# Optimization experiments

Hardware: AMD Instinct MI355X
Metric: run time of the kernel (lower is better)

## Reference

```python
import jax, jax.numpy as jnp
import numpy as np

D = 768          # hidden_size
M = 8            # num_patchmerges
B = 16
S = 2048         # non-CLF tokens


def setup_inputs() -> dict:
    key = jax.random.key(0)
    ks = jax.random.split(key, 12)
    std = 0.02
    tokens = jax.random.normal(ks[0], (B, 1 + S, D), dtype=jnp.float32)
    lengths = jnp.maximum(jax.random.randint(ks[1], (B,), 0, S), 1).astype(jnp.int64)
    # PatchMerger: learned queries + layernorm params
    q = jax.random.normal(ks[2], (M, D), dtype=jnp.float32) * std
    ln_scale = jnp.ones((D,), dtype=jnp.float32)
    ln_bias = jnp.zeros((D,), dtype=jnp.float32)
    # mlp1: Linear(3D, D) -> GELU -> Linear(D, D)
    w1a = jax.random.normal(ks[3], (3 * D, D), dtype=jnp.float32) * std
    b1a = jnp.zeros((D,), dtype=jnp.float32)
    w2a = jax.random.normal(ks[4], (D, D), dtype=jnp.float32) * std
    b2a = jnp.zeros((D,), dtype=jnp.float32)
    # mlp2: Linear((1+M)D, D) -> GELU -> Linear(D, D)
    w1b = jax.random.normal(ks[5], ((1 + M) * D, D), dtype=jnp.float32) * std
    b1b = jnp.zeros((D,), dtype=jnp.float32)
    w2b = jax.random.normal(ks[6], (D, D), dtype=jnp.float32) * std
    b2b = jnp.zeros((D,), dtype=jnp.float32)
    return dict(tokens=tokens, lengths=lengths, q=q, ln_scale=ln_scale,
                ln_bias=ln_bias, w1a=w1a, b1a=b1a, w2a=w2a, b2a=b2a,
                w1b=w1b, b1b=b1b, w2b=w2b, b2b=b2b)


def _hpmlp(x, w1, b1, w2, b2):
    h = jax.nn.gelu(x @ w1 + b1, approximate=False)  # dropout=0 -> identity
    return h @ w2 + b2


def _layernorm(x, scale, bias, eps=1e-5):
    mu = jnp.mean(x, axis=-1, keepdims=True)
    var = jnp.var(x, axis=-1, keepdims=True)
    return (x - mu) * jax.lax.rsqrt(var + eps) * scale + bias


def reference(tokens, lengths, q, ln_scale, ln_bias,
              w1a, b1a, w2a, b2a, w1b, b1b, w2b, b2b):
    clf = tokens[:, 0]            # [B, D]
    x = tokens[:, 1:]             # [B, S, D]
    mask = jnp.arange(S)[None, :] < lengths[:, None]   # [B, S]
    mf = mask[..., None].astype(x.dtype)

    # fixed path: masked mean / max / min over valid tokens
    denom = lengths.astype(x.dtype)[:, None]
    mean_p = jnp.sum(x * mf, axis=1) / denom
    max_p = jnp.max(jnp.where(mask[..., None], x, -jnp.inf), axis=1)
    min_p = jnp.min(jnp.where(mask[..., None], x, jnp.inf), axis=1)
    pooled_trad = jnp.concatenate([mean_p, max_p, min_p], axis=-1)  # [B, 3D]
    out_fixed = _hpmlp(pooled_trad, w1a, b1a, w2a, b2a)

    # learned path: PatchMerger (masked attention from M learned queries)
    xn = _layernorm(x, ln_scale, ln_bias)
    scores = jnp.einsum('md,bsd->bms', q, xn) / jnp.sqrt(jnp.asarray(D, x.dtype))
    scores = jnp.where(mask[:, None, :], scores, -jnp.inf)
    attn = jax.nn.softmax(scores, axis=-1)                # [B, M, S]
    merged = jnp.einsum('bms,bsd->bmd', attn, x)          # [B, M, D]
    pooled_learn = jnp.concatenate([merged.reshape(B, M * D), clf], axis=-1)
    out_learn = _hpmlp(pooled_learn, w1b, b1b, w2b, b2b)

    return jnp.concatenate([out_fixed, out_learn], axis=-1)  # [B, 2D]
```

## Files before the change

### kernel.cpp

```cpp
#include <hip/hip_runtime.h>
#include <math.h>

#define SD 768
#define SB 16
#define SM 8
#define SS 2048
#define TOK_ROW 2049
#define NEG_INF (-__builtin_inff())

#define OFF_PPOOL   0
#define OFF_PO      1179648
#define OFF_PML     4325376
#define OFF_PTRAD   4333568
#define OFF_PLEARN  4370432
#define OFF_P1A     4481024
#define OFF_P1B     4702208
#define OFF_P2A     5390336
#define OFF_P2B     5464064

__device__ __forceinline__ int clen(int v) { return v < 1 ? 1 : (v > SS ? SS : v); }

__global__ __launch_bounds__(256, 1) void k1_flash(
    const float* __restrict__ tokens, const int* __restrict__ lengths,
    const float* __restrict__ q, const float* __restrict__ lns,
    const float* __restrict__ lnb, float* __restrict__ ppool,
    float* __restrict__ pO, float* __restrict__ pml) {
  int c = blockIdx.x, b = blockIdx.y;
  int len = clen(lengths[b]);
  int c0 = c * 64;
  if (c0 >= len) return;
  int tid = threadIdx.x, w = tid >> 6, lane = tid & 63;
  int mm = lane & 7;

  __shared__ float pool_lds[4][3][SD];
  __shared__ float O_lds[SM][SD];
  __shared__ float l_lds[4][8];

  float4 qr[8][3];
  float qs1sel, qbsel;
  {
    float4 l4[3], lb4[3];
    #pragma unroll
    for (int g = 0; g < 3; ++g) {
      l4[g] = *(const float4*)(lns + g * 256 + lane * 4);
      lb4[g] = *(const float4*)(lnb + g * 256 + lane * 4);
    }
    float qs1r[8], qbr[8];
    #pragma unroll
    for (int m = 0; m < 8; ++m) {
      float s1 = 0.f, sb = 0.f;
      #pragma unroll
      for (int g = 0; g < 3; ++g) {
        float4 qv = *(const float4*)(q + m * SD + g * 256 + lane * 4);
        float4 qs;
        qs.x = qv.x * l4[g].x; qs.y = qv.y * l4[g].y;
        qs.z = qv.z * l4[g].z; qs.w = qv.w * l4[g].w;
        qr[m][g] = qs;
        s1 += qs.x + qs.y + qs.z + qs.w;
        sb += qv.x * lb4[g].x + qv.y * lb4[g].y + qv.z * lb4[g].z + qv.w * lb4[g].w;
      }
      #pragma unroll
      for (int o = 32; o; o >>= 1) { s1 += __shfl_xor(s1, o, 64); sb += __shfl_xor(sb, o, 64); }
      qs1r[m] = s1; qbr[m] = sb;
    }
    qs1sel = qs1r[0]; qbsel = qbr[0];
    #pragma unroll
    for (int m = 1; m < 8; ++m) {
      qs1sel = (mm == m) ? qs1r[m] : qs1sel;
      qbsel = (mm == m) ? qbr[m] : qbsel;
    }
  }

  float psum[12], pmax[12], pmin[12];
  #pragma unroll
  for (int j = 0; j < 12; ++j) { psum[j] = 0.f; pmax[j] = NEG_INF; pmin[j] = -NEG_INF; }
  float O[8][12];
  #pragma unroll
  for (int m = 0; m < 8; ++m)
    #pragma unroll
    for (int j = 0; j < 12; ++j) O[m][j] = 0.f;
  float lacc = 0.f;

  int srow = c0 + w * 16;
  int smax = len - srow; if (smax > 16) smax = 16; if (smax < 0) smax = 0;
  const float* xrow = tokens + ((size_t)b * TOK_ROW + 1 + srow) * SD;

  float4 a0v = {}, a1v = {}, a2v = {}, b0v = {}, b1v = {}, b2v = {};
  if (smax > 0) {
    a0v = *(const float4*)(xrow + lane * 4);
    a1v = *(const float4*)(xrow + 256 + lane * 4);
    a2v = *(const float4*)(xrow + 512 + lane * 4);
  }
  if (smax > 1) {
    const float* xq = xrow + SD;
    b0v = *(const float4*)(xq + lane * 4);
    b1v = *(const float4*)(xq + 256 + lane * 4);
    b2v = *(const float4*)(xq + 512 + lane * 4);
  }
  for (int i = 0; i < smax; ++i) {
    float4 x0 = a0v, x1 = a1v, x2 = a2v;
    a0v = b0v; a1v = b1v; a2v = b2v;
    if (i + 2 < smax) {
      const float* xq = xrow + (size_t)(i + 2) * SD;
      b0v = *(const float4*)(xq + lane * 4);
      b1v = *(const float4*)(xq + 256 + lane * 4);
      b2v = *(const float4*)(xq + 512 + lane * 4);
    }
    float xv[12] = {x0.x, x0.y, x0.z, x0.w, x1.x, x1.y, x1.z, x1.w,
                    x2.x, x2.y, x2.z, x2.w};
    float s1 = 0.f, s2 = 0.f;
    #pragma unroll
    for (int j = 0; j < 12; ++j) {
      float v = xv[j];
      psum[j] += v;
      pmax[j] = fmaxf(pmax[j], v);
      pmin[j] = fminf(pmin[j], v);
      s1 += v;
      s2 += v * v;
    }
    float d[8];
    #pragma unroll
    for (int m = 0; m < 8; ++m) {
      float4 a0 = qr[m][0], a1 = qr[m][1], a2 = qr[m][2];
      d[m] = a0.x * xv[0] + a0.y * xv[1] + a0.z * xv[2] + a0.w * xv[3]
           + a1.x * xv[4] + a1.y * xv[5] + a1.z * xv[6] + a1.w * xv[7]
           + a2.x * xv[8] + a2.y * xv[9] + a2.z * xv[10] + a2.w * xv[11];
    }
    #pragma unroll
    for (int o = 1; o <= 4; o <<= 1)
      #pragma unroll
      for (int m = 0; m < 8; ++m) d[m] += __shfl_xor(d[m], o, 64);
    float u = d[0];
    #pragma unroll
    for (int m = 1; m < 8; ++m) u = (mm == m) ? d[m] : u;
    #pragma unroll
    for (int o = 8; o <= 32; o <<= 1) {
      u += __shfl_xor(u, o, 64);
      s1 += __shfl_xor(s1, o, 64);
      s2 += __shfl_xor(s2, o, 64);
    }
    #pragma unroll
    for (int o = 1; o <= 4; o <<= 1) { s1 += __shfl_xor(s1, o, 64); s2 += __shfl_xor(s2, o, 64); }
    float mu = s1 * (1.f / 768.f);
    float var = s2 * (1.f / 768.f) - mu * mu;
    float rstd = rsqrtf(var + 1e-5f);
    float sc = (rstd * u - rstd * mu * qs1sel + qbsel) * 0.03608439182435161f;
    float p = __expf(sc);
    lacc += p;
    float pm[8];
    #pragma unroll
    for (int mi = 0; mi < 8; ++mi) pm[mi] = __shfl(p, (lane & 56) | mi, 64);
    #pragma unroll
    for (int m = 0; m < 8; ++m)
      #pragma unroll
      for (int j = 0; j < 12; ++j) O[m][j] += pm[m] * xv[j];
  }

  if (lane < 8) l_lds[w][lane] = lacc;
  #pragma unroll
  for (int g = 0; g < 3; ++g) {
    int dd = g * 256 + lane * 4;
    *(float4*)&pool_lds[w][0][dd] = make_float4(psum[g*4], psum[g*4+1], psum[g*4+2], psum[g*4+3]);
    *(float4*)&pool_lds[w][1][dd] = make_float4(pmax[g*4], pmax[g*4+1], pmax[g*4+2], pmax[g*4+3]);
    *(float4*)&pool_lds[w][2][dd] = make_float4(pmin[g*4], pmin[g*4+1], pmin[g*4+2], pmin[g*4+3]);
  }
  __syncthreads();
  if (tid < 8)
    pml[(size_t)(c * SB + b) * 8 + tid] =
        l_lds[0][tid] + l_lds[1][tid] + l_lds[2][tid] + l_lds[3][tid];

  #pragma unroll
  for (int r = 0; r < 4; ++r) {
    if (w == r) {
      #pragma unroll
      for (int m = 0; m < 8; ++m)
        #pragma unroll
        for (int g = 0; g < 3; ++g) {
          int dd = g * 256 + lane * 4;
          float4 mine = make_float4(O[m][g*4], O[m][g*4+1], O[m][g*4+2], O[m][g*4+3]);
          if (r == 0) {
            *(float4*)&O_lds[m][dd] = mine;
          } else {
            float4 cur = *(float4*)&O_lds[m][dd];
            cur.x += mine.x; cur.y += mine.y; cur.z += mine.z; cur.w += mine.w;
            *(float4*)&O_lds[m][dd] = cur;
          }
        }
    }
    __syncthreads();
  }

  size_t obase = (size_t)(c * SB + b) * 6144;
  const float* of = &O_lds[0][0];
  for (int j = tid * 4; j < 6144; j += 1024)
    *(float4*)&pO[obase + j] = *(const float4*)&of[j];

  size_t pbase = (size_t)(c * SB + b) * 2304;
  for (int j4 = tid * 4; j4 < 2304; j4 += 1024) {
    int stat = j4 / SD, dd = j4 - stat * SD;
    float4 v0 = *(float4*)&pool_lds[0][stat][dd];
    float4 v1 = *(float4*)&pool_lds[1][stat][dd];
    float4 v2 = *(float4*)&pool_lds[2][stat][dd];
    float4 v3 = *(float4*)&pool_lds[3][stat][dd];
    float4 r;
    if (stat == 0) {
      r.x = v0.x + v1.x + v2.x + v3.x; r.y = v0.y + v1.y + v2.y + v3.y;
      r.z = v0.z + v1.z + v2.z + v3.z; r.w = v0.w + v1.w + v2.w + v3.w;
    } else if (stat == 1) {
      r.x = fmaxf(fmaxf(v0.x, v1.x), fmaxf(v2.x, v3.x));
      r.y = fmaxf(fmaxf(v0.y, v1.y), fmaxf(v2.y, v3.y));
      r.z = fmaxf(fmaxf(v0.z, v1.z), fmaxf(v2.z, v3.z));
      r.w = fmaxf(fmaxf(v0.w, v1.w), fmaxf(v2.w, v3.w));
    } else {
      r.x = fminf(fminf(v0.x, v1.x), fminf(v2.x, v3.x));
      r.y = fminf(fminf(v0.y, v1.y), fminf(v2.y, v3.y));
      r.z = fminf(fminf(v0.z, v1.z), fminf(v2.z, v3.z));
      r.w = fminf(fminf(v0.w, v1.w), fminf(v2.w, v3.w));
    }
    *(float4*)&ppool[pbase + j4] = r;
  }
}

__global__ void k_combine(const float* __restrict__ ppool, const float* __restrict__ pO,
                          const float* __restrict__ pml, const float* __restrict__ tokens,
                          const int* __restrict__ lengths,
                          float* __restrict__ ptrad, float* __restrict__ plearn) {
  int tile = blockIdx.x, b = blockIdx.y;
  int len = clen(lengths[b]);
  int nv = (len + 63) >> 6;
  int tid = threadIdx.x;
  __shared__ float l_sh[32][8];
  __shared__ float Linv_lds[8];
  for (int t = tid; t < nv * 8; t += 256)
    l_sh[t >> 3][t & 7] = pml[(size_t)((t >> 3) * SB + b) * 8 + (t & 7)];
  __syncthreads();
  if (tid < 8) {
    float L = 0.f;
    for (int cc = 0; cc < nv; ++cc) L += l_sh[cc][tid];
    Linv_lds[tid] = 1.f / L;
  }
  __syncthreads();
  #pragma unroll
  for (int k = 0; k < 4; ++k) {
    int jj = tile * 1024 + k * 256 + tid;
    if (jj < 2304) {
      int stat = jj / SD;
      const float* pp = ppool + jj + (size_t)b * 2304;
      if (stat == 0) {
        float a0 = 0.f, a1 = 0.f, a2 = 0.f, a3 = 0.f;
        int cc = 0;
        for (; cc + 4 <= nv; cc += 4) {
          a0 += pp[(size_t)(cc    ) * SB * 2304];
          a1 += pp[(size_t)(cc + 1) * SB * 2304];
          a2 += pp[(size_t)(cc + 2) * SB * 2304];
          a3 += pp[(size_t)(cc + 3) * SB * 2304];
        }
        for (; cc < nv; ++cc) a0 += pp[(size_t)cc * SB * 2304];
        ptrad[b * 2304 + jj] = ((a0 + a1) + (a2 + a3)) / (float)len;
      } else if (stat == 1) {
        float a0 = NEG_INF, a1 = NEG_INF, a2 = NEG_INF, a3 = NEG_INF;
        int cc = 0;
        for (; cc + 4 <= nv; cc += 4) {
          a0 = fmaxf(a0, pp[(size_t)(cc    ) * SB * 2304]);
          a1 = fmaxf(a1, pp[(size_t)(cc + 1) * SB * 2304]);
          a2 = fmaxf(a2, pp[(size_t)(cc + 2) * SB * 2304]);
          a3 = fmaxf(a3, pp[(size_t)(cc + 3) * SB * 2304]);
        }
        for (; cc < nv; ++cc) a0 = fmaxf(a0, pp[(size_t)cc * SB * 2304]);
        ptrad[b * 2304 + jj] = fmaxf(fmaxf(a0, a1), fmaxf(a2, a3));
      } else {
        float a0 = -NEG_INF, a1 = -NEG_INF, a2 = -NEG_INF, a3 = -NEG_INF;
        int cc = 0;
        for (; cc + 4 <= nv; cc += 4) {
          a0 = fminf(a0, pp[(size_t)(cc    ) * SB * 2304]);
          a1 = fminf(a1, pp[(size_t)(cc + 1) * SB * 2304]);
          a2 = fminf(a2, pp[(size_t)(cc + 2) * SB * 2304]);
          a3 = fminf(a3, pp[(size_t)(cc + 3) * SB * 2304]);
        }
        for (; cc < nv; ++cc) a0 = fminf(a0, pp[(size_t)cc * SB * 2304]);
        ptrad[b * 2304 + jj] = fminf(fminf(a0, a1), fminf(a2, a3));
      }
    } else if (jj < 8448) {
      int t = jj - 2304;
      int m = t / SD;
      const float* po = pO + t + (size_t)b * 6144;
      float a0 = 0.f, a1 = 0.f, a2 = 0.f, a3 = 0.f;
      float a4 = 0.f, a5 = 0.f, a6 = 0.f, a7 = 0.f;
      int cc = 0;
      for (; cc + 8 <= nv; cc += 8) {
        a0 += po[(size_t)(cc    ) * SB * 6144];
        a1 += po[(size_t)(cc + 1) * SB * 6144];
        a2 += po[(size_t)(cc + 2) * SB * 6144];
        a3 += po[(size_t)(cc + 3) * SB * 6144];
        a4 += po[(size_t)(cc + 4) * SB * 6144];
        a5 += po[(size_t)(cc + 5) * SB * 6144];
        a6 += po[(size_t)(cc + 6) * SB * 6144];
        a7 += po[(size_t)(cc + 7) * SB * 6144];
      }
      for (; cc < nv; ++cc) a0 += po[(size_t)cc * SB * 6144];
      plearn[b * 6912 + t] = (((a0 + a1) + (a2 + a3)) + ((a4 + a5) + (a6 + a7))) * Linv_lds[m];
    } else {
      int dd = jj - 8448;
      plearn[b * 6912 + 6144 + dd] = tokens[(size_t)b * TOK_ROW * SD + dd];
    }
  }
}

__global__ __launch_bounds__(256) void gemm_partial(
    const float* __restrict__ XA, const float* __restrict__ WA, int ktA, float* __restrict__ PA,
    const float* __restrict__ XB, const float* __restrict__ WB, float* __restrict__ PB) {
  int nt = blockIdx.x, ky = blockIdx.y;
  const float *X, *W; float* P; int kt, ktN;
  if (ky < ktA) { X = XA; W = WA; P = PA; kt = ky; ktN = ktA; }
  else { X = XB; W = WB; P = PB; kt = ky - ktA; ktN = gridDim.y - ktA; }
  int K = ktN * 128;
  int k0 = kt * 128;
  __shared__ __align__(16) float xt[128 * 20];
  __shared__ float red[4][64][17];
  int tid = threadIdx.x;
  int kk = tid & 127, half = tid >> 7;
  #pragma unroll
  for (int u = 0; u < 8; ++u) {
    int b2 = half * 8 + u;
    xt[kk * 20 + b2] = X[b2 * K + k0 + kk];
  }
  __syncthreads();
  int w = tid >> 6, lane = tid & 63;
  int n = nt * 64 + lane;
  float acc[16];
  #pragma unroll
  for (int b2 = 0; b2 < 16; ++b2) acc[b2] = 0.f;
  const float* Wp = W + (size_t)k0 * SD + n;
  #pragma unroll 8
  for (int kj = 0; kj < 32; ++kj) {
    int k = w + kj * 4;
    float wv = Wp[(size_t)k * SD];
    const float4* xr = reinterpret_cast<const float4*>(xt + k * 20);
    float4 a0 = xr[0], a1 = xr[1], a2 = xr[2], a3 = xr[3];
    acc[0] += wv * a0.x; acc[1] += wv * a0.y; acc[2] += wv * a0.z; acc[3] += wv * a0.w;
    acc[4] += wv * a1.x; acc[5] += wv * a1.y; acc[6] += wv * a1.z; acc[7] += wv * a1.w;
    acc[8] += wv * a2.x; acc[9] += wv * a2.y; acc[10] += wv * a2.z; acc[11] += wv * a2.w;
    acc[12] += wv * a3.x; acc[13] += wv * a3.y; acc[14] += wv * a3.z; acc[15] += wv * a3.w;
  }
  #pragma unroll
  for (int b2 = 0; b2 < 16; ++b2) red[w][lane][b2] = acc[b2];
  __syncthreads();
  for (int i = tid; i < 1024; i += 256) {
    int nn = i & 63, b2 = i >> 6;
    float r = red[0][nn][b2] + red[1][nn][b2] + red[2][nn][b2] + red[3][nn][b2];
    P[(size_t)(kt * 16 + b2) * SD + nt * 64 + nn] = r;
  }
}

template <int NP>
__device__ __forceinline__ void stage_gelu(const float* __restrict__ P1,
                                           const float* __restrict__ bias,
                                           float* __restrict__ xt, int k0, int tid) {
  int kk = tid & 127, half = tid >> 7;
  #pragma unroll
  for (int u = 0; u < 8; ++u) {
    int b2 = half * 8 + u;
    float r = bias[k0 + kk];
    const float* p = P1 + (size_t)b2 * SD + k0 + kk;
    #pragma unroll
    for (int kt2 = 0; kt2 < NP; ++kt2) r += p[(size_t)kt2 * 12288];
    xt[kk * 20 + b2] = r * 0.5f * (1.f + erff(r * 0.70710678118654752f));
  }
}

__global__ __launch_bounds__(256) void gemm2_gelu(
    const float* __restrict__ P1A, const float* __restrict__ b1a,
    const float* __restrict__ W2A, float* __restrict__ P2A,
    const float* __restrict__ P1B, const float* __restrict__ b1b,
    const float* __restrict__ W2B, float* __restrict__ P2B) {
  int nt = blockIdx.x, ky = blockIdx.y;
  __shared__ __align__(16) float xt[128 * 20];
  __shared__ float red[4][64][17];
  int tid = threadIdx.x;
  const float* W; float* P2; int kt;
  if (ky < 6) { kt = ky; W = W2A; P2 = P2A; stage_gelu<18>(P1A, b1a, xt, kt * 128, tid); }
  else { kt = ky - 6; W = W2B; P2 = P2B; stage_gelu<54>(P1B, b1b, xt, kt * 128, tid); }
  int k0 = kt * 128;
  __syncthreads();
  int w = tid >> 6, lane = tid & 63;
  int n = nt * 64 + lane;
  float acc[16];
  #pragma unroll
  for (int b2 = 0; b2 < 16; ++b2) acc[b2] = 0.f;
  const float* Wp = W + (size_t)k0 * SD + n;
  #pragma unroll 8
  for (int kj = 0; kj < 32; ++kj) {
    int k = w + kj * 4;
    float wv = Wp[(size_t)k * SD];
    const float4* xr = reinterpret_cast<const float4*>(xt + k * 20);
    float4 a0 = xr[0], a1 = xr[1], a2 = xr[2], a3 = xr[3];
    acc[0] += wv * a0.x; acc[1] += wv * a0.y; acc[2] += wv * a0.z; acc[3] += wv * a0.w;
    acc[4] += wv * a1.x; acc[5] += wv * a1.y; acc[6] += wv * a1.z; acc[7] += wv * a1.w;
    acc[8] += wv * a2.x; acc[9] += wv * a2.y; acc[10] += wv * a2.z; acc[11] += wv * a2.w;
    acc[12] += wv * a3.x; acc[13] += wv * a3.y; acc[14] += wv * a3.z; acc[15] += wv * a3.w;
  }
  #pragma unroll
  for (int b2 = 0; b2 < 16; ++b2) red[w][lane][b2] = acc[b2];
  __syncthreads();
  for (int i = tid; i < 1024; i += 256) {
    int nn = i & 63, b2 = i >> 6;
    float r = red[0][nn][b2] + red[1][nn][b2] + red[2][nn][b2] + red[3][nn][b2];
    P2[(size_t)(kt * 16 + b2) * SD + nt * 64 + nn] = r;
  }
}

__global__ void final_reduce(const float* __restrict__ P2A, const float* __restrict__ b2a,
                             const float* __restrict__ P2B, const float* __restrict__ b2b,
                             float* __restrict__ out) {
  int y = blockIdx.y;
  const float* P = y ? P2B : P2A;
  const float* bias = y ? b2b : b2a;
  int j = blockIdx.x * 256 + threadIdx.x;
  float r = bias[j % SD];
  #pragma unroll
  for (int kt = 0; kt < 6; ++kt) r += P[kt * 12288 + j];
  int b = j / SD, nn = j - b * SD;
  out[b * 1536 + y * SD + nn] = r;
}

extern "C" void kernel_launch(void* const* d_in, const int* in_sizes, int n_in,
                              void* d_out, int out_size, void* d_ws, size_t ws_size,
                              hipStream_t stream) {
  const float* tokens = (const float*)d_in[0];
  const int* lengths  = (const int*)d_in[1];
  const float* q      = (const float*)d_in[2];
  const float* lns    = (const float*)d_in[3];
  const float* lnb    = (const float*)d_in[4];
  const float* w1a    = (const float*)d_in[5];
  const float* b1a    = (const float*)d_in[6];
  const float* w2a    = (const float*)d_in[7];
  const float* b2a    = (const float*)d_in[8];
  const float* w1b    = (const float*)d_in[9];
  const float* b1b    = (const float*)d_in[10];
  const float* w2b    = (const float*)d_in[11];
  const float* b2b    = (const float*)d_in[12];
  float* ws  = (float*)d_ws;
  float* out = (float*)d_out;

  float* ppool  = ws + OFF_PPOOL;
  float* pO     = ws + OFF_PO;
  float* pml    = ws + OFF_PML;
  float* ptrad  = ws + OFF_PTRAD;
  float* plearn = ws + OFF_PLEARN;
  float* p1a    = ws + OFF_P1A;
  float* p1b    = ws + OFF_P1B;
  float* p2a    = ws + OFF_P2A;
  float* p2b    = ws + OFF_P2B;

  k1_flash<<<dim3(32, 16), 256, 0, stream>>>(tokens, lengths, q, lns, lnb, ppool, pO, pml);
  k_combine<<<dim3(9, 16), 256, 0, stream>>>(ppool, pO, pml, tokens, lengths, ptrad, plearn);
  gemm_partial<<<dim3(12, 72), 256, 0, stream>>>(ptrad, w1a, 18, p1a, plearn, w1b, p1b);
  gemm2_gelu<<<dim3(12, 12), 256, 0, stream>>>(p1a, b1a, w2a, p2a, p1b, b1b, w2b, p2b);
  final_reduce<<<dim3(48, 2), 256, 0, stream>>>(p2a, b2a, p2b, b2b, out);
}
```

Measured before the change: 266.8 us.

## Split flash kernel into score and accumulate passes to raise occupancy

The flash pooling kernel now makes two passes over its tokens. The first pass computes the stats and softmax weights and stores the weights in LDS. The second pass re-reads the tokens and accumulates the weighted sums, so the O accumulators are no longer live while the score math runs. This cuts register pressure, which allows launch_bounds 3 and shares LDS between the pool and O buffers. Chunk size drops from 64 to 32 tokens, doubling the grid and the partial buffers that k_combine reduces, and each token is read twice (the second read likely from cache).

```diff
diff --git a/kernel.cpp b/kernel.cpp
--- a/kernel.cpp
+++ b/kernel.cpp
@@ -9,31 +9,31 @@
 #define NEG_INF (-__builtin_inff())
 
 #define OFF_PPOOL   0
-#define OFF_PO      1179648
-#define OFF_PML     4325376
-#define OFF_PTRAD   4333568
-#define OFF_PLEARN  4370432
-#define OFF_P1A     4481024
-#define OFF_P1B     4702208
-#define OFF_P2A     5390336
-#define OFF_P2B     5464064
+#define OFF_PO      2359296
+#define OFF_PML     8650752
+#define OFF_PTRAD   8658944
+#define OFF_PLEARN  8695808
+#define OFF_P1A     8806400
+#define OFF_P1B     9027584
+#define OFF_P2A     9691136
+#define OFF_P2B     9764864
 
 __device__ __forceinline__ int clen(int v) { return v < 1 ? 1 : (v > SS ? SS : v); }
 
-__global__ __launch_bounds__(256, 1) void k1_flash(
+__global__ __launch_bounds__(256, 3) void k1_flash(
     const float* __restrict__ tokens, const int* __restrict__ lengths,
     const float* __restrict__ q, const float* __restrict__ lns,
     const float* __restrict__ lnb, float* __restrict__ ppool,
     float* __restrict__ pO, float* __restrict__ pml) {
   int c = blockIdx.x, b = blockIdx.y;
   int len = clen(lengths[b]);
-  int c0 = c * 64;
+  int c0 = c * 32;
   if (c0 >= len) return;
   int tid = threadIdx.x, w = tid >> 6, lane = tid & 63;
   int mm = lane & 7;
 
-  __shared__ float pool_lds[4][3][SD];
-  __shared__ float O_lds[SM][SD];
+  __shared__ float buf[4][3][SD];
+  __shared__ float p_lds[4][8][8];
   __shared__ float l_lds[4][8];
 
   float4 qr[8][3];
@@ -74,38 +74,17 @@
   float psum[12], pmax[12], pmin[12];
   #pragma unroll
   for (int j = 0; j < 12; ++j) { psum[j] = 0.f; pmax[j] = NEG_INF; pmin[j] = -NEG_INF; }
-  float O[8][12];
-  #pragma unroll
-  for (int m = 0; m < 8; ++m)
-    #pragma unroll
-    for (int j = 0; j < 12; ++j) O[m][j] = 0.f;
   float lacc = 0.f;
 
-  int srow = c0 + w * 16;
-  int smax = len - srow; if (smax > 16) smax = 16; if (smax < 0) smax = 0;
+  int srow = c0 + w * 8;
+  int smax = len - srow; if (smax > 8) smax = 8; if (smax < 0) smax = 0;
   const float* xrow = tokens + ((size_t)b * TOK_ROW + 1 + srow) * SD;
 
-  float4 a0v = {}, a1v = {}, a2v = {}, b0v = {}, b1v = {}, b2v = {};
-  if (smax > 0) {
-    a0v = *(const float4*)(xrow + lane * 4);
-    a1v = *(const float4*)(xrow + 256 + lane * 4);
-    a2v = *(const float4*)(xrow + 512 + lane * 4);
-  }
-  if (smax > 1) {
-    const float* xq = xrow + SD;
-    b0v = *(const float4*)(xq + lane * 4);
-    b1v = *(const float4*)(xq + 256 + lane * 4);
-    b2v = *(const float4*)(xq + 512 + lane * 4);
-  }
   for (int i = 0; i < smax; ++i) {
-    float4 x0 = a0v, x1 = a1v, x2 = a2v;
-    a0v = b0v; a1v = b1v; a2v = b2v;
-    if (i + 2 < smax) {
-      const float* xq = xrow + (size_t)(i + 2) * SD;
-      b0v = *(const float4*)(xq + lane * 4);
-      b1v = *(const float4*)(xq + 256 + lane * 4);
-      b2v = *(const float4*)(xq + 512 + lane * 4);
-    }
+    const float* xp = xrow + (size_t)i * SD;
+    float4 x0 = *(const float4*)(xp + lane * 4);
+    float4 x1 = *(const float4*)(xp + 256 + lane * 4);
+    float4 x2 = *(const float4*)(xp + 512 + lane * 4);
     float xv[12] = {x0.x, x0.y, x0.z, x0.w, x1.x, x1.y, x1.z, x1.w,
                     x2.x, x2.y, x2.z, x2.w};
     float s1 = 0.f, s2 = 0.f;
@@ -127,9 +106,12 @@
            + a2.x * xv[8] + a2.y * xv[9] + a2.z * xv[10] + a2.w * xv[11];
     }
     #pragma unroll
-    for (int o = 1; o <= 4; o <<= 1)
+    for (int o = 1; o <= 4; o <<= 1) {
       #pragma unroll
       for (int m = 0; m < 8; ++m) d[m] += __shfl_xor(d[m], o, 64);
+      s1 += __shfl_xor(s1, o, 64);
+      s2 += __shfl_xor(s2, o, 64);
+    }
     float u = d[0];
     #pragma unroll
     for (int m = 1; m < 8; ++m) u = (mm == m) ? d[m] : u;
@@ -139,69 +121,32 @@
       s1 += __shfl_xor(s1, o, 64);
       s2 += __shfl_xor(s2, o, 64);
     }
-    #pragma unroll
-    for (int o = 1; o <= 4; o <<= 1) { s1 += __shfl_xor(s1, o, 64); s2 += __shfl_xor(s2, o, 64); }
     float mu = s1 * (1.f / 768.f);
     float var = s2 * (1.f / 768.f) - mu * mu;
     float rstd = rsqrtf(var + 1e-5f);
     float sc = (rstd * u - rstd * mu * qs1sel + qbsel) * 0.03608439182435161f;
     float p = __expf(sc);
     lacc += p;
-    float pm[8];
-    #pragma unroll
-    for (int mi = 0; mi < 8; ++mi) pm[mi] = __shfl(p, (lane & 56) | mi, 64);
-    #pragma unroll
-    for (int m = 0; m < 8; ++m)
-      #pragma unroll
-      for (int j = 0; j < 12; ++j) O[m][j] += pm[m] * xv[j];
-  }
-
-  if (lane < 8) l_lds[w][lane] = lacc;
+    if (lane < 8) p_lds[w][i][lane] = p;
+  }
+
   #pragma unroll
   for (int g = 0; g < 3; ++g) {
     int dd = g * 256 + lane * 4;
-    *(float4*)&pool_lds[w][0][dd] = make_float4(psum[g*4], psum[g*4+1], psum[g*4+2], psum[g*4+3]);
-    *(float4*)&pool_lds[w][1][dd] = make_float4(pmax[g*4], pmax[g*4+1], pmax[g*4+2], pmax[g*4+3]);
-    *(float4*)&pool_lds[w][2][dd] = make_float4(pmin[g*4], pmin[g*4+1], pmin[g*4+2], pmin[g*4+3]);
-  }
-  __syncthreads();
-  if (tid < 8)
-    pml[(size_t)(c * SB + b) * 8 + tid] =
-        l_lds[0][tid] + l_lds[1][tid] + l_lds[2][tid] + l_lds[3][tid];
-
-  #pragma unroll
-  for (int r = 0; r < 4; ++r) {
-    if (w == r) {
-      #pragma unroll
-      for (int m = 0; m < 8; ++m)
-        #pragma unroll
-        for (int g = 0; g < 3; ++g) {
-          int dd = g * 256 + lane * 4;
-          float4 mine = make_float4(O[m][g*4], O[m][g*4+1], O[m][g*4+2], O[m][g*4+3]);
-          if (r == 0) {
-            *(float4*)&O_lds[m][dd] = mine;
-          } else {
-            float4 cur = *(float4*)&O_lds[m][dd];
-            cur.x += mine.x; cur.y += mine.y; cur.z += mine.z; cur.w += mine.w;
-            *(float4*)&O_lds[m][dd] = cur;
-          }
-        }
-    }
-    __syncthreads();
-  }
-
-  size_t obase = (size_t)(c * SB + b) * 6144;
-  const float* of = &O_lds[0][0];
-  for (int j = tid * 4; j < 6144; j += 1024)
-    *(float4*)&pO[obase + j] = *(const float4*)&of[j];
+    *(float4*)&buf[w][0][dd] = make_float4(psum[g*4], psum[g*4+1], psum[g*4+2], psum[g*4+3]);
+    *(float4*)&buf[w][1][dd] = make_float4(pmax[g*4], pmax[g*4+1], pmax[g*4+2], pmax[g*4+3]);
+    *(float4*)&buf[w][2][dd] = make_float4(pmin[g*4], pmin[g*4+1], pmin[g*4+2], pmin[g*4+3]);
+  }
+  if (lane < 8) l_lds[w][lane] = lacc;
+  __syncthreads();
 
   size_t pbase = (size_t)(c * SB + b) * 2304;
   for (int j4 = tid * 4; j4 < 2304; j4 += 1024) {
     int stat = j4 / SD, dd = j4 - stat * SD;
-    float4 v0 = *(float4*)&pool_lds[0][stat][dd];
-    float4 v1 = *(float4*)&pool_lds[1][stat][dd];
-    float4 v2 = *(float4*)&pool_lds[2][stat][dd];
-    float4 v3 = *(float4*)&pool_lds[3][stat][dd];
+    float4 v0 = *(float4*)&buf[0][stat][dd];
+    float4 v1 = *(float4*)&buf[1][stat][dd];
+    float4 v2 = *(float4*)&buf[2][stat][dd];
+    float4 v3 = *(float4*)&buf[3][stat][dd];
     float4 r;
     if (stat == 0) {
       r.x = v0.x + v1.x + v2.x + v3.x; r.y = v0.y + v1.y + v2.y + v3.y;
@@ -219,6 +164,73 @@
     }
     *(float4*)&ppool[pbase + j4] = r;
   }
+  if (tid < 8)
+    pml[(size_t)(c * SB + b) * 8 + tid] =
+        l_lds[0][tid] + l_lds[1][tid] + l_lds[2][tid] + l_lds[3][tid];
+  __syncthreads();
+
+  float O[8][12];
+  #pragma unroll
+  for (int m = 0; m < 8; ++m)
+    #pragma unroll
+    for (int j = 0; j < 12; ++j) O[m][j] = 0.f;
+  float4 a0v = {}, a1v = {}, a2v = {}, b0v = {}, b1v = {}, b2v = {};
+  if (smax > 0) {
+    a0v = *(const float4*)(xrow + lane * 4);
+    a1v = *(const float4*)(xrow + 256 + lane * 4);
+    a2v = *(const float4*)(xrow + 512 + lane * 4);
+  }
+  if (smax > 1) {
+    const float* xq = xrow + SD;
+    b0v = *(const float4*)(xq + lane * 4);
+    b1v = *(const float4*)(xq + 256 + lane * 4);
+    b2v = *(const float4*)(xq + 512 + lane * 4);
+  }
+  for (int i = 0; i < smax; ++i) {
+    float4 x0 = a0v, x1 = a1v, x2 = a2v;
+    a0v = b0v; a1v = b1v; a2v = b2v;
+    if (i + 2 < smax) {
+      const float* xq = xrow + (size_t)(i + 2) * SD;
+      b0v = *(const float4*)(xq + lane * 4);
+      b1v = *(const float4*)(xq + 256 + lane * 4);
+      b2v = *(const float4*)(xq + 512 + lane * 4);
+    }
+    float xv[12] = {x0.x, x0.y, x0.z, x0.w, x1.x, x1.y, x1.z, x1.w,
+                    x2.x, x2.y, x2.z, x2.w};
+    const float4* pr = (const float4*)&p_lds[w][i][0];
+    float4 pa = pr[0], pb = pr[1];
+    float pm[8] = {pa.x, pa.y, pa.z, pa.w, pb.x, pb.y, pb.z, pb.w};
+    #pragma unroll
+    for (int m = 0; m < 8; ++m)
+      #pragma unroll
+      for (int j = 0; j < 12; ++j) O[m][j] += pm[m] * xv[j];
+  }
+
+  float* Ol = &buf[0][0][0];
+  #pragma unroll
+  for (int r = 0; r < 4; ++r) {
+    if (w == r) {
+      #pragma unroll
+      for (int m = 0; m < 8; ++m)
+        #pragma unroll
+        for (int g = 0; g < 3; ++g) {
+          int dd = m * SD + g * 256 + lane * 4;
+          float4 mine = make_float4(O[m][g*4], O[m][g*4+1], O[m][g*4+2], O[m][g*4+3]);
+          if (r == 0) {
+            *(float4*)&Ol[dd] = mine;
+          } else {
+            float4 cur = *(float4*)&Ol[dd];
+            cur.x += mine.x; cur.y += mine.y; cur.z += mine.z; cur.w += mine.w;
+            *(float4*)&Ol[dd] = cur;
+          }
+        }
+    }
+    __syncthreads();
+  }
+
+  size_t obase = (size_t)(c * SB + b) * 6144;
+  for (int j = tid * 4; j < 6144; j += 1024)
+    *(float4*)&pO[obase + j] = *(const float4*)&Ol[j];
 }
 
 __global__ void k_combine(const float* __restrict__ ppool, const float* __restrict__ pO,
@@ -227,9 +239,9 @@
                           float* __restrict__ ptrad, float* __restrict__ plearn) {
   int tile = blockIdx.x, b = blockIdx.y;
   int len = clen(lengths[b]);
-  int nv = (len + 63) >> 6;
+  int nv = (len + 31) >> 5;
   int tid = threadIdx.x;
-  __shared__ float l_sh[32][8];
+  __shared__ float l_sh[64][8];
   __shared__ float Linv_lds[8];
   for (int t = tid; t < nv * 8; t += 256)
     l_sh[t >> 3][t & 7] = pml[(size_t)((t >> 3) * SB + b) * 8 + (t & 7)];
@@ -452,7 +464,7 @@
   float* p2a    = ws + OFF_P2A;
   float* p2b    = ws + OFF_P2B;
 
-  k1_flash<<<dim3(32, 16), 256, 0, stream>>>(tokens, lengths, q, lns, lnb, ppool, pO, pml);
+  k1_flash<<<dim3(64, 16), 256, 0, stream>>>(tokens, lengths, q, lns, lnb, ppool, pO, pml);
   k_combine<<<dim3(9, 16), 256, 0, stream>>>(ppool, pO, pml, tokens, lengths, ptrad, plearn);
   gemm_partial<<<dim3(12, 72), 256, 0, stream>>>(ptrad, w1a, 18, p1a, plearn, w1b, p1b);
   gemm2_gelu<<<dim3(12, 12), 256, 0, stream>>>(p1a, b1a, w2a, p2a, p1b, b1b, w2b, p2b);
```

After: 263.3 us. About the same (-1.3%).

## Split flash kernel into score pass and accumulation pass to cut register pressure

Applied to the files above, without the earlier changes.

Restructures k1_flash into two passes over each wave's 16 rows. The first pass computes pooling stats, layernorm and softmax weights two rows at a time, storing the weights in LDS. The second pass re-reads the rows and accumulates the weighted output, so the stats and O accumulators are never live together. LDS buffers are merged and launch bounds raised to two blocks per SM to improve occupancy, at the cost of reading each token row from global memory twice.

```diff
diff --git a/kernel.cpp b/kernel.cpp
--- a/kernel.cpp
+++ b/kernel.cpp
@@ -20,7 +20,7 @@
 
 __device__ __forceinline__ int clen(int v) { return v < 1 ? 1 : (v > SS ? SS : v); }
 
-__global__ __launch_bounds__(256, 1) void k1_flash(
+__global__ __launch_bounds__(256, 2) void k1_flash(
     const float* __restrict__ tokens, const int* __restrict__ lengths,
     const float* __restrict__ q, const float* __restrict__ lns,
     const float* __restrict__ lnb, float* __restrict__ ppool,
@@ -32,8 +32,8 @@
   int tid = threadIdx.x, w = tid >> 6, lane = tid & 63;
   int mm = lane & 7;
 
-  __shared__ float pool_lds[4][3][SD];
-  __shared__ float O_lds[SM][SD];
+  __shared__ float buf[4][3][SD];
+  __shared__ float p_lds[4][16][8];
   __shared__ float l_lds[4][8];
 
   float4 qr[8][3];
@@ -74,18 +74,184 @@
   float psum[12], pmax[12], pmin[12];
   #pragma unroll
   for (int j = 0; j < 12; ++j) { psum[j] = 0.f; pmax[j] = NEG_INF; pmin[j] = -NEG_INF; }
-  float O[8][12];
-  #pragma unroll
-  for (int m = 0; m < 8; ++m)
-    #pragma unroll
-    for (int j = 0; j < 12; ++j) O[m][j] = 0.f;
   float lacc = 0.f;
 
   int srow = c0 + w * 16;
   int smax = len - srow; if (smax > 16) smax = 16; if (smax < 0) smax = 0;
   const float* xrow = tokens + ((size_t)b * TOK_ROW + 1 + srow) * SD;
 
-  float4 a0v = {}, a1v = {}, a2v = {}, b0v = {}, b1v = {}, b2v = {};
+  float4 A0={},A1={},A2={}, B0={},B1={},B2={}, C0={},C1={},C2={}, D0={},D1={},D2={};
+  if (smax > 0) {
+    A0 = *(const float4*)(xrow + lane * 4);
+    A1 = *(const float4*)(xrow + 256 + lane * 4);
+    A2 = *(const float4*)(xrow + 512 + lane * 4);
+  }
+  if (smax > 1) {
+    const float* p = xrow + SD;
+    B0 = *(const float4*)(p + lane * 4);
+    B1 = *(const float4*)(p + 256 + lane * 4);
+    B2 = *(const float4*)(p + 512 + lane * 4);
+  }
+  if (smax > 2) {
+    const float* p = xrow + 2 * SD;
+    C0 = *(const float4*)(p + lane * 4);
+    C1 = *(const float4*)(p + 256 + lane * 4);
+    C2 = *(const float4*)(p + 512 + lane * 4);
+  }
+  if (smax > 3) {
+    const float* p = xrow + 3 * SD;
+    D0 = *(const float4*)(p + lane * 4);
+    D1 = *(const float4*)(p + 256 + lane * 4);
+    D2 = *(const float4*)(p + 512 + lane * 4);
+  }
+
+  int i = 0;
+  for (; i + 1 < smax; i += 2) {
+    float4 x0=A0,x1=A1,x2=A2, y0=B0,y1=B1,y2=B2;
+    A0=C0;A1=C1;A2=C2; B0=D0;B1=D1;B2=D2;
+    if (i + 4 < smax) {
+      const float* p = xrow + (size_t)(i + 4) * SD;
+      C0 = *(const float4*)(p + lane * 4);
+      C1 = *(const float4*)(p + 256 + lane * 4);
+      C2 = *(const float4*)(p + 512 + lane * 4);
+    }
+    if (i + 5 < smax) {
+      const float* p = xrow + (size_t)(i + 5) * SD;
+      D0 = *(const float4*)(p + lane * 4);
+      D1 = *(const float4*)(p + 256 + lane * 4);
+      D2 = *(const float4*)(p + 512 + lane * 4);
+    }
+    float xv[12] = {x0.x,x0.y,x0.z,x0.w, x1.x,x1.y,x1.z,x1.w, x2.x,x2.y,x2.z,x2.w};
+    float yv[12] = {y0.x,y0.y,y0.z,y0.w, y1.x,y1.y,y1.z,y1.w, y2.x,y2.y,y2.z,y2.w};
+    float s1a=0.f, s2a=0.f, s1b=0.f, s2b=0.f;
+    #pragma unroll
+    for (int j = 0; j < 12; ++j) {
+      float vx = xv[j], vy = yv[j];
+      psum[j] += vx + vy;
+      pmax[j] = fmaxf(pmax[j], fmaxf(vx, vy));
+      pmin[j] = fminf(pmin[j], fminf(vx, vy));
+      s1a += vx; s2a += vx * vx;
+      s1b += vy; s2b += vy * vy;
+    }
+    float da[8], db[8];
+    #pragma unroll
+    for (int m = 0; m < 8; ++m) {
+      float4 a0 = qr[m][0], a1 = qr[m][1], a2 = qr[m][2];
+      da[m] = a0.x*xv[0]+a0.y*xv[1]+a0.z*xv[2]+a0.w*xv[3]
+            + a1.x*xv[4]+a1.y*xv[5]+a1.z*xv[6]+a1.w*xv[7]
+            + a2.x*xv[8]+a2.y*xv[9]+a2.z*xv[10]+a2.w*xv[11];
+      db[m] = a0.x*yv[0]+a0.y*yv[1]+a0.z*yv[2]+a0.w*yv[3]
+            + a1.x*yv[4]+a1.y*yv[5]+a1.z*yv[6]+a1.w*yv[7]
+            + a2.x*yv[8]+a2.y*yv[9]+a2.z*yv[10]+a2.w*yv[11];
+    }
+    #pragma unroll
+    for (int o = 1; o <= 4; o <<= 1) {
+      #pragma unroll
+      for (int m = 0; m < 8; ++m) { da[m] += __shfl_xor(da[m], o, 64); db[m] += __shfl_xor(db[m], o, 64); }
+      s1a += __shfl_xor(s1a, o, 64); s2a += __shfl_xor(s2a, o, 64);
+      s1b += __shfl_xor(s1b, o, 64); s2b += __shfl_xor(s2b, o, 64);
+    }
+    float ua = da[0], ub = db[0];
+    #pragma unroll
+    for (int m = 1; m < 8; ++m) { ua = (mm == m) ? da[m] : ua; ub = (mm == m) ? db[m] : ub; }
+    #pragma unroll
+    for (int o = 8; o <= 32; o <<= 1) {
+      ua += __shfl_xor(ua, o, 64); ub += __shfl_xor(ub, o, 64);
+      s1a += __shfl_xor(s1a, o, 64); s2a += __shfl_xor(s2a, o, 64);
+      s1b += __shfl_xor(s1b, o, 64); s2b += __shfl_xor(s2b, o, 64);
+    }
+    float mua = s1a * (1.f/768.f), mub = s1b * (1.f/768.f);
+    float rsta = rsqrtf(s2a * (1.f/768.f) - mua*mua + 1e-5f);
+    float rstb = rsqrtf(s2b * (1.f/768.f) - mub*mub + 1e-5f);
+    float sca = (rsta * ua - rsta * mua * qs1sel + qbsel) * 0.03608439182435161f;
+    float scb = (rstb * ub - rstb * mub * qs1sel + qbsel) * 0.03608439182435161f;
+    float pa = __expf(sca), pb = __expf(scb);
+    lacc += pa + pb;
+    if (lane < 8) { p_lds[w][i][lane] = pa; p_lds[w][i + 1][lane] = pb; }
+  }
+  if (i < smax) {
+    float xv[12] = {A0.x,A0.y,A0.z,A0.w, A1.x,A1.y,A1.z,A1.w, A2.x,A2.y,A2.z,A2.w};
+    float s1 = 0.f, s2 = 0.f;
+    #pragma unroll
+    for (int j = 0; j < 12; ++j) {
+      float v = xv[j];
+      psum[j] += v; pmax[j] = fmaxf(pmax[j], v); pmin[j] = fminf(pmin[j], v);
+      s1 += v; s2 += v * v;
+    }
+    float d[8];
+    #pragma unroll
+    for (int m = 0; m < 8; ++m) {
+      float4 a0 = qr[m][0], a1 = qr[m][1], a2 = qr[m][2];
+      d[m] = a0.x*xv[0]+a0.y*xv[1]+a0.z*xv[2]+a0.w*xv[3]
+           + a1.x*xv[4]+a1.y*xv[5]+a1.z*xv[6]+a1.w*xv[7]
+           + a2.x*xv[8]+a2.y*xv[9]+a2.z*xv[10]+a2.w*xv[11];
+    }
+    #pragma unroll
+    for (int o = 1; o <= 4; o <<= 1) {
+      #pragma unroll
+      for (int m = 0; m < 8; ++m) d[m] += __shfl_xor(d[m], o, 64);
+      s1 += __shfl_xor(s1, o, 64); s2 += __shfl_xor(s2, o, 64);
+    }
+    float u = d[0];
+    #pragma unroll
+    for (int m = 1; m < 8; ++m) u = (mm == m) ? d[m] : u;
+    #pragma unroll
+    for (int o = 8; o <= 32; o <<= 1) {
+      u += __shfl_xor(u, o, 64); s1 += __shfl_xor(s1, o, 64); s2 += __shfl_xor(s2, o, 64);
+    }
+    float mu = s1 * (1.f/768.f);
+    float rstd = rsqrtf(s2 * (1.f/768.f) - mu*mu + 1e-5f);
+    float sc = (rstd * u - rstd * mu * qs1sel + qbsel) * 0.03608439182435161f;
+    float p = __expf(sc);
+    lacc += p;
+    if (lane < 8) p_lds[w][i][lane] = p;
+  }
+
+  #pragma unroll
+  for (int g = 0; g < 3; ++g) {
+    int dd = g * 256 + lane * 4;
+    *(float4*)&buf[w][0][dd] = make_float4(psum[g*4], psum[g*4+1], psum[g*4+2], psum[g*4+3]);
+    *(float4*)&buf[w][1][dd] = make_float4(pmax[g*4], pmax[g*4+1], pmax[g*4+2], pmax[g*4+3]);
+    *(float4*)&buf[w][2][dd] = make_float4(pmin[g*4], pmin[g*4+1], pmin[g*4+2], pmin[g*4+3]);
+  }
+  if (lane < 8) l_lds[w][lane] = lacc;
+  __syncthreads();
+
+  size_t pbase = (size_t)(c * SB + b) * 2304;
+  for (int j4 = tid * 4; j4 < 2304; j4 += 1024) {
+    int stat = j4 / SD, dd = j4 - stat * SD;
+    float4 v0 = *(float4*)&buf[0][stat][dd];
+    float4 v1 = *(float4*)&buf[1][stat][dd];
+    float4 v2 = *(float4*)&buf[2][stat][dd];
+    float4 v3 = *(float4*)&buf[3][stat][dd];
+    float4 r;
+    if (stat == 0) {
+      r.x = v0.x+v1.x+v2.x+v3.x; r.y = v0.y+v1.y+v2.y+v3.y;
+      r.z = v0.z+v1.z+v2.z+v3.z; r.w = v0.w+v1.w+v2.w+v3.w;
+    } else if (stat == 1) {
+      r.x = fmaxf(fmaxf(v0.x,v1.x), fmaxf(v2.x,v3.x));
+      r.y = fmaxf(fmaxf(v0.y,v1.y), fmaxf(v2.y,v3.y));
+      r.z = fmaxf(fmaxf(v0.z,v1.z), fmaxf(v2.z,v3.z));
+      r.w = fmaxf(fmaxf(v0.w,v1.w), fmaxf(v2.w,v3.w));
+    } else {
+      r.x = fminf(fminf(v0.x,v1.x), fminf(v2.x,v3.x));
+      r.y = fminf(fminf(v0.y,v1.y), fminf(v2.y,v3.y));
+      r.z = fminf(fminf(v0.z,v1.z), fminf(v2.z,v3.z));
+      r.w = fminf(fminf(v0.w,v1.w), fminf(v2.w,v3.w));
+    }
+    *(float4*)&ppool[pbase + j4] = r;
+  }
+  if (tid < 8)
+    pml[(size_t)(c * SB + b) * 8 + tid] =
+        l_lds[0][tid] + l_lds[1][tid] + l_lds[2][tid] + l_lds[3][tid];
+  __syncthreads();
+
+  float O[8][12];
+  #pragma unroll
+  for (int m = 0; m < 8; ++m)
+    #pragma unroll
+    for (int j = 0; j < 12; ++j) O[m][j] = 0.f;
+  float4 a0v={},a1v={},a2v={}, b0v={},b1v={},b2v={};
   if (smax > 0) {
     a0v = *(const float4*)(xrow + lane * 4);
     a1v = *(const float4*)(xrow + 256 + lane * 4);
@@ -97,78 +263,26 @@
     b1v = *(const float4*)(xq + 256 + lane * 4);
     b2v = *(const float4*)(xq + 512 + lane * 4);
   }
-  for (int i = 0; i < smax; ++i) {
+  for (int k = 0; k < smax; ++k) {
     float4 x0 = a0v, x1 = a1v, x2 = a2v;
     a0v = b0v; a1v = b1v; a2v = b2v;
-    if (i + 2 < smax) {
-      const float* xq = xrow + (size_t)(i + 2) * SD;
+    if (k + 2 < smax) {
+      const float* xq = xrow + (size_t)(k + 2) * SD;
       b0v = *(const float4*)(xq + lane * 4);
       b1v = *(const float4*)(xq + 256 + lane * 4);
       b2v = *(const float4*)(xq + 512 + lane * 4);
     }
-    float xv[12] = {x0.x, x0.y, x0.z, x0.w, x1.x, x1.y, x1.z, x1.w,
-                    x2.x, x2.y, x2.z, x2.w};
-    float s1 = 0.f, s2 = 0.f;
-    #pragma unroll
-    for (int j = 0; j < 12; ++j) {
-      float v = xv[j];
-      psum[j] += v;
-      pmax[j] = fmaxf(pmax[j], v);
-      pmin[j] = fminf(pmin[j], v);
-      s1 += v;
-      s2 += v * v;
-    }
-    float d[8];
-    #pragma unroll
-    for (int m = 0; m < 8; ++m) {
-      float4 a0 = qr[m][0], a1 = qr[m][1], a2 = qr[m][2];
-      d[m] = a0.x * xv[0] + a0.y * xv[1] + a0.z * xv[2] + a0.w * xv[3]
-           + a1.x * xv[4] + a1.y * xv[5] + a1.z * xv[6] + a1.w * xv[7]
-           + a2.x * xv[8] + a2.y * xv[9] + a2.z * xv[10] + a2.w * xv[11];
-    }
-    #pragma unroll
-    for (int o = 1; o <= 4; o <<= 1)
-      #pragma unroll
-      for (int m = 0; m < 8; ++m) d[m] += __shfl_xor(d[m], o, 64);
-    float u = d[0];
-    #pragma unroll
-    for (int m = 1; m < 8; ++m) u = (mm == m) ? d[m] : u;
-    #pragma unroll
-    for (int o = 8; o <= 32; o <<= 1) {
-      u += __shfl_xor(u, o, 64);
-      s1 += __shfl_xor(s1, o, 64);
-      s2 += __shfl_xor(s2, o, 64);
-    }
-    #pragma unroll
-    for (int o = 1; o <= 4; o <<= 1) { s1 += __shfl_xor(s1, o, 64); s2 += __shfl_xor(s2, o, 64); }
-    float mu = s1 * (1.f / 768.f);
-    float var = s2 * (1.f / 768.f) - mu * mu;
-    float rstd = rsqrtf(var + 1e-5f);
-    float sc = (rstd * u - rstd * mu * qs1sel + qbsel) * 0.03608439182435161f;
-    float p = __expf(sc);
-    lacc += p;
-    float pm[8];
-    #pragma unroll
-    for (int mi = 0; mi < 8; ++mi) pm[mi] = __shfl(p, (lane & 56) | mi, 64);
+    float xv[12] = {x0.x,x0.y,x0.z,x0.w, x1.x,x1.y,x1.z,x1.w, x2.x,x2.y,x2.z,x2.w};
+    const float4* pr = (const float4*)&p_lds[w][k][0];
+    float4 pa = pr[0], pb = pr[1];
+    float pm[8] = {pa.x, pa.y, pa.z, pa.w, pb.x, pb.y, pb.z, pb.w};
     #pragma unroll
     for (int m = 0; m < 8; ++m)
       #pragma unroll
       for (int j = 0; j < 12; ++j) O[m][j] += pm[m] * xv[j];
   }
 
-  if (lane < 8) l_lds[w][lane] = lacc;
-  #pragma unroll
-  for (int g = 0; g < 3; ++g) {
-    int dd = g * 256 + lane * 4;
-    *(float4*)&pool_lds[w][0][dd] = make_float4(psum[g*4], psum[g*4+1], psum[g*4+2], psum[g*4+3]);
-    *(float4*)&pool_lds[w][1][dd] = make_float4(pmax[g*4], pmax[g*4+1], pmax[g*4+2], pmax[g*4+3]);
-    *(float4*)&pool_lds[w][2][dd] = make_float4(pmin[g*4], pmin[g*4+1], pmin[g*4+2], pmin[g*4+3]);
-  }
-  __syncthreads();
-  if (tid < 8)
-    pml[(size_t)(c * SB + b) * 8 + tid] =
-        l_lds[0][tid] + l_lds[1][tid] + l_lds[2][tid] + l_lds[3][tid];
-
+  float* Ol = &buf[0][0][0];
   #pragma unroll
   for (int r = 0; r < 4; ++r) {
     if (w == r) {
@@ -176,14 +290,14 @@
       for (int m = 0; m < 8; ++m)
         #pragma unroll
         for (int g = 0; g < 3; ++g) {
-          int dd = g * 256 + lane * 4;
+          int dd = m * SD + g * 256 + lane * 4;
           float4 mine = make_float4(O[m][g*4], O[m][g*4+1], O[m][g*4+2], O[m][g*4+3]);
           if (r == 0) {
-            *(float4*)&O_lds[m][dd] = mine;
+            *(float4*)&Ol[dd] = mine;
           } else {
-            float4 cur = *(float4*)&O_lds[m][dd];
+            float4 cur = *(float4*)&Ol[dd];
             cur.x += mine.x; cur.y += mine.y; cur.z += mine.z; cur.w += mine.w;
-            *(float4*)&O_lds[m][dd] = cur;
+            *(float4*)&Ol[dd] = cur;
           }
         }
     }
@@ -191,34 +305,8 @@
   }
 
   size_t obase = (size_t)(c * SB + b) * 6144;
-  const float* of = &O_lds[0][0];
   for (int j = tid * 4; j < 6144; j += 1024)
-    *(float4*)&pO[obase + j] = *(const float4*)&of[j];
-
-  size_t pbase = (size_t)(c * SB + b) * 2304;
-  for (int j4 = tid * 4; j4 < 2304; j4 += 1024) {
-    int stat = j4 / SD, dd = j4 - stat * SD;
-    float4 v0 = *(float4*)&pool_lds[0][stat][dd];
-    float4 v1 = *(float4*)&pool_lds[1][stat][dd];
-    float4 v2 = *(float4*)&pool_lds[2][stat][dd];
-    float4 v3 = *(float4*)&pool_lds[3][stat][dd];
-    float4 r;
-    if (stat == 0) {
-      r.x = v0.x + v1.x + v2.x + v3.x; r.y = v0.y + v1.y + v2.y + v3.y;
-      r.z = v0.z + v1.z + v2.z + v3.z; r.w = v0.w + v1.w + v2.w + v3.w;
-    } else if (stat == 1) {
-      r.x = fmaxf(fmaxf(v0.x, v1.x), fmaxf(v2.x, v3.x));
-      r.y = fmaxf(fmaxf(v0.y, v1.y), fmaxf(v2.y, v3.y));
-      r.z = fmaxf(fmaxf(v0.z, v1.z), fmaxf(v2.z, v3.z));
-      r.w = fmaxf(fmaxf(v0.w, v1.w), fmaxf(v2.w, v3.w));
-    } else {
-      r.x = fminf(fminf(v0.x, v1.x), fminf(v2.x, v3.x));
-      r.y = fminf(fminf(v0.y, v1.y), fminf(v2.y, v3.y));
-      r.z = fminf(fminf(v0.z, v1.z), fminf(v2.z, v3.z));
-      r.w = fminf(fminf(v0.w, v1.w), fminf(v2.w, v3.w));
-    }
-    *(float4*)&ppool[pbase + j4] = r;
-  }
+    *(float4*)&pO[obase + j] = *(const float4*)&Ol[j];
 }
 
 __global__ void k_combine(const float* __restrict__ ppool, const float* __restrict__ pO,
```

After: 246.7 us. 1.08x faster.
